# Performance work log

Measured on AMD Instinct MI355X. Metric: run time of the kernel, lower is better.

## Reference

```python
import jax, jax.numpy as jnp
import numpy as np

S = 2048      # seq_len (prefill, empty cache)
H = 32        # num query heads
HKV = 8       # num kv heads
D = 128       # head_dim
G = H // HKV  # GQA group size
SCALE = 0.08838834764831845  # 1/sqrt(D)


def setup_inputs() -> dict:
    key = jax.random.key(0)
    k1, k2, k3 = jax.random.split(key, 3)
    return {
        "query": jax.random.normal(k1, (S, H * D), dtype=jnp.float32),
        "key": jax.random.normal(k2, (S, HKV * D), dtype=jnp.float32),
        "value": jax.random.normal(k3, (S, HKV * D), dtype=jnp.float32),
    }


def reference(query, key, value):
    # [S, H, D] -> [HKV, G, S, D]; head h attends to kv head h // G,
    # equivalent to torch repeat_interleave on kv heads without materializing copies.
    q = query.reshape(S, H, D).transpose(1, 0, 2).reshape(HKV, G, S, D)
    k = key.reshape(S, HKV, D).transpose(1, 0, 2)    # [HKV, S, D]
    v = value.reshape(S, HKV, D).transpose(1, 0, 2)  # [HKV, S, D]

    scores = jnp.einsum('hgqd,htd->hgqt', q, k) * SCALE  # [HKV, G, S, S]
    causal = jnp.tril(jnp.ones((S, S), dtype=bool))      # j <= i allowed
    scores = jnp.where(causal, scores, jnp.finfo(scores.dtype).min)
    attn = jax.nn.softmax(scores, axis=-1)
    out = jnp.einsum('hgqt,htd->hgqd', attn, v)          # [HKV, G, S, D]
    out = out.reshape(H, S, D).transpose(1, 0, 2).reshape(S, H * D)
    return out
```

## Files before the change

kernel.cpp:

```cpp
#include <hip/hip_runtime.h>
#include <hip/hip_bf16.h>

#define S_LEN 2048
#define NH    32
#define NKV   8
#define HD    128
#define QBLK  128
#define KVBLK 64
#define NWAVE 8
#define KST   136
#define VST   68
#define PST   72

typedef __bf16 bf16x8   __attribute__((ext_vector_type(8)));
typedef __bf16 bf16x4_t __attribute__((ext_vector_type(4)));
typedef float  f32x4    __attribute__((ext_vector_type(4)));

__global__ __launch_bounds__(512, 4)
void sdpa_fwd(const float* __restrict__ Q, const float* __restrict__ K,
              const float* __restrict__ V, float* __restrict__ O)
{
    __shared__ __align__(16) unsigned short Klds_u[KVBLK * KST];
    __shared__ __align__(16) unsigned short Vt_u[HD * VST];
    __shared__ __align__(16) unsigned short P_u[QBLK * PST];
    __bf16* Klds = (__bf16*)Klds_u;
    __bf16* Vt   = (__bf16*)Vt_u;
    __bf16* Pl   = (__bf16*)P_u;

    const int qt   = (int)gridDim.x - 1 - (int)blockIdx.x;
    const int h    = blockIdx.y;
    const int hkv  = h >> 2;
    const int q0   = qt * QBLK;
    const int tid  = threadIdx.x;
    const int wv   = tid >> 6;
    const int lane = tid & 63;
    const int lr   = lane & 15;
    const int lg   = lane >> 4;
    const int qrow0 = q0 + wv * 16;

    const float NEG_INF = -__builtin_inff();
    const float QSCALE  = (float)(0.08838834764831845 * 1.4426950408889634);

    bf16x8 qf[4];
    {
        const float* qp = Q + (size_t)(qrow0 + lr) * (NH * HD) + h * HD + lg * 8;
        #pragma unroll
        for (int f = 0; f < 4; ++f) {
            float4 a = *(const float4*)(qp + f * 32);
            float4 b = *(const float4*)(qp + f * 32 + 4);
            bf16x8 t;
            t[0] = (__bf16)(a.x * QSCALE); t[1] = (__bf16)(a.y * QSCALE);
            t[2] = (__bf16)(a.z * QSCALE); t[3] = (__bf16)(a.w * QSCALE);
            t[4] = (__bf16)(b.x * QSCALE); t[5] = (__bf16)(b.y * QSCALE);
            t[6] = (__bf16)(b.z * QSCALE); t[7] = (__bf16)(b.w * QSCALE);
            qf[f] = t;
        }
    }

    f32x4 o[8];
    #pragma unroll
    for (int dt = 0; dt < 8; ++dt) o[dt] = (f32x4){0.f, 0.f, 0.f, 0.f};
    float m_r[4] = {NEG_INF, NEG_INF, NEG_INF, NEG_INF};
    float l_r[4] = {0.f, 0.f, 0.f, 0.f};

    const int kb_end = q0 + QBLK - KVBLK;
    for (int kb = 0; kb <= kb_end; kb += KVBLK) {
        __syncthreads();
        #pragma unroll
        for (int it = 0; it < 4; ++it) {
            int idx = (it * 512 + tid) * 4;
            int row = idx >> 7, col = idx & 127;
            float4 k4 = *(const float4*)(K + (size_t)(kb + row) * (NKV * HD) + hkv * HD + col);
            bf16x4_t kb4;
            kb4[0] = (__bf16)k4.x; kb4[1] = (__bf16)k4.y;
            kb4[2] = (__bf16)k4.z; kb4[3] = (__bf16)k4.w;
            *(bf16x4_t*)&Klds[row * KST + col] = kb4;
        }
        #pragma unroll
        for (int it = 0; it < 4; ++it) {
            int task = it * 512 + tid;
            int col = task & 127, rg = task >> 7;
            const float* vp = V + (size_t)(kb + rg * 4) * (NKV * HD) + hkv * HD + col;
            bf16x4_t vb;
            vb[0] = (__bf16)vp[0];
            vb[1] = (__bf16)vp[NKV * HD];
            vb[2] = (__bf16)vp[2 * NKV * HD];
            vb[3] = (__bf16)vp[3 * NKV * HD];
            *(bf16x4_t*)&Vt[col * VST + rg * 4] = vb;
        }
        __syncthreads();

        if (kb > qrow0 + 15) continue;

        f32x4 s[4];
        #pragma unroll
        for (int t = 0; t < 4; ++t) {
            f32x4 acc = (f32x4){0.f, 0.f, 0.f, 0.f};
            #pragma unroll
            for (int f = 0; f < 4; ++f) {
                bf16x8 kf = *(bf16x8*)&Klds[(t * 16 + lr) * KST + f * 32 + lg * 8];
                acc = __builtin_amdgcn_mfma_f32_16x16x32_bf16(qf[f], kf, acc, 0, 0, 0);
            }
            s[t] = acc;
        }

        const bool needmask = (kb + KVBLK - 1 > qrow0);
        float sv[4][4];
        float mt[4] = {NEG_INF, NEG_INF, NEG_INF, NEG_INF};
        #pragma unroll
        for (int t = 0; t < 4; ++t)
            #pragma unroll
            for (int r = 0; r < 4; ++r) {
                float val = s[t][r];
                if (needmask && (kb + t * 16 + lr) > (qrow0 + lg * 4 + r)) val = NEG_INF;
                sv[t][r] = val;
                mt[r] = fmaxf(mt[r], val);
            }
        #pragma unroll
        for (int r = 0; r < 4; ++r) {
            #pragma unroll
            for (int off = 1; off < 16; off <<= 1)
                mt[r] = fmaxf(mt[r], __shfl_xor(mt[r], off));
        }
        float alpha[4];
        #pragma unroll
        for (int r = 0; r < 4; ++r) {
            float mn  = fmaxf(m_r[r], mt[r]);
            alpha[r]  = __builtin_amdgcn_exp2f(m_r[r] - mn);
            m_r[r]    = mn;
            l_r[r]   *= alpha[r];
        }
        #pragma unroll
        for (int dt = 0; dt < 8; ++dt) {
            o[dt][0] *= alpha[0]; o[dt][1] *= alpha[1];
            o[dt][2] *= alpha[2]; o[dt][3] *= alpha[3];
        }
        #pragma unroll
        for (int t = 0; t < 4; ++t)
            #pragma unroll
            for (int r = 0; r < 4; ++r) {
                float p = __builtin_amdgcn_exp2f(sv[t][r] - m_r[r]);
                l_r[r] += p;
                Pl[(wv * 16 + lg * 4 + r) * PST + t * 16 + lr] = (__bf16)p;
            }
        #pragma unroll
        for (int ks = 0; ks < 2; ++ks) {
            bf16x8 pf = *(bf16x8*)&Pl[(wv * 16 + lr) * PST + ks * 32 + lg * 8];
            #pragma unroll
            for (int dt = 0; dt < 8; ++dt) {
                bf16x8 vf = *(bf16x8*)&Vt[(dt * 16 + lr) * VST + ks * 32 + lg * 8];
                o[dt] = __builtin_amdgcn_mfma_f32_16x16x32_bf16(pf, vf, o[dt], 0, 0, 0);
            }
        }
    }

    float inv[4];
    #pragma unroll
    for (int r = 0; r < 4; ++r) {
        float lsum = l_r[r];
        #pragma unroll
        for (int off = 1; off < 16; off <<= 1)
            lsum += __shfl_xor(lsum, off);
        inv[r] = 1.0f / lsum;
    }
    #pragma unroll
    for (int dt = 0; dt < 8; ++dt)
        #pragma unroll
        for (int r = 0; r < 4; ++r) {
            int qrow = qrow0 + lg * 4 + r;
            O[(size_t)qrow * (NH * HD) + h * HD + dt * 16 + lr] = o[dt][r] * inv[r];
        }
}

extern "C" void kernel_launch(void* const* d_in, const int* in_sizes, int n_in,
                              void* d_out, int out_size, void* d_ws, size_t ws_size,
                              hipStream_t stream)
{
    const float* Q = (const float*)d_in[0];
    const float* K = (const float*)d_in[1];
    const float* V = (const float*)d_in[2];
    float* O = (float*)d_out;
    dim3 grid(S_LEN / QBLK, NH);
    sdpa_fwd<<<grid, 512, 0, stream>>>(Q, K, V, O);
}
```

Measured before the change: 395.1 us.

## Pair causal query tiles per block and prefetch next KV tile into registers

Each block now handles two 64-row query chunks, one from the start and one from the end of the sequence, so every block has about the same causal work instead of the triangular imbalance of the old grid. It also prefetches the next K/V tile from global memory into registers while the current tile is computed, then converts and writes it to LDS after a barrier. The cost is extra registers for the prefetch buffers (16 float4-equivalents per thread), which may reduce occupancy under launch_bounds(512,4). The first-chunk waves idle through most of the loop iterations.

```diff
diff --git a/kernel.cpp b/kernel.cpp
--- a/kernel.cpp
+++ b/kernel.cpp
@@ -5,9 +5,7 @@
 #define NH    32
 #define NKV   8
 #define HD    128
-#define QBLK  128
 #define KVBLK 64
-#define NWAVE 8
 #define KST   136
 #define VST   68
 #define PST   72
@@ -22,21 +20,21 @@
 {
     __shared__ __align__(16) unsigned short Klds_u[KVBLK * KST];
     __shared__ __align__(16) unsigned short Vt_u[HD * VST];
-    __shared__ __align__(16) unsigned short P_u[QBLK * PST];
+    __shared__ __align__(16) unsigned short P_u[128 * PST];
     __bf16* Klds = (__bf16*)Klds_u;
     __bf16* Vt   = (__bf16*)Vt_u;
     __bf16* Pl   = (__bf16*)P_u;
 
-    const int qt   = (int)gridDim.x - 1 - (int)blockIdx.x;
+    const int p    = blockIdx.x;
     const int h    = blockIdx.y;
     const int hkv  = h >> 2;
-    const int q0   = qt * QBLK;
     const int tid  = threadIdx.x;
     const int wv   = tid >> 6;
     const int lane = tid & 63;
     const int lr   = lane & 15;
     const int lg   = lane >> 4;
-    const int qrow0 = q0 + wv * 16;
+    const int qrow0 = (wv < 4) ? (64 * p + 16 * wv)
+                               : (S_LEN - 64 * (p + 1) + 16 * (wv - 4));
 
     const float NEG_INF = -__builtin_inff();
     const float QSCALE  = (float)(0.08838834764831845 * 1.4426950408889634);
@@ -63,95 +61,122 @@
     float m_r[4] = {NEG_INF, NEG_INF, NEG_INF, NEG_INF};
     float l_r[4] = {0.f, 0.f, 0.f, 0.f};
 
-    const int kb_end = q0 + QBLK - KVBLK;
-    for (int kb = 0; kb <= kb_end; kb += KVBLK) {
-        __syncthreads();
+    float4 kreg[4];
+    float  vreg[16];
+
+    auto issue_loads = [&](int kb) {
         #pragma unroll
         for (int it = 0; it < 4; ++it) {
             int idx = (it * 512 + tid) * 4;
             int row = idx >> 7, col = idx & 127;
-            float4 k4 = *(const float4*)(K + (size_t)(kb + row) * (NKV * HD) + hkv * HD + col);
-            bf16x4_t kb4;
-            kb4[0] = (__bf16)k4.x; kb4[1] = (__bf16)k4.y;
-            kb4[2] = (__bf16)k4.z; kb4[3] = (__bf16)k4.w;
-            *(bf16x4_t*)&Klds[row * KST + col] = kb4;
+            kreg[it] = *(const float4*)(K + (size_t)(kb + row) * (NKV * HD) + hkv * HD + col);
         }
         #pragma unroll
         for (int it = 0; it < 4; ++it) {
             int task = it * 512 + tid;
             int col = task & 127, rg = task >> 7;
             const float* vp = V + (size_t)(kb + rg * 4) * (NKV * HD) + hkv * HD + col;
+            vreg[it * 4 + 0] = vp[0];
+            vreg[it * 4 + 1] = vp[NKV * HD];
+            vreg[it * 4 + 2] = vp[2 * NKV * HD];
+            vreg[it * 4 + 3] = vp[3 * NKV * HD];
+        }
+    };
+    auto write_lds = [&]() {
+        #pragma unroll
+        for (int it = 0; it < 4; ++it) {
+            int idx = (it * 512 + tid) * 4;
+            int row = idx >> 7, col = idx & 127;
+            bf16x4_t kb4;
+            kb4[0] = (__bf16)kreg[it].x; kb4[1] = (__bf16)kreg[it].y;
+            kb4[2] = (__bf16)kreg[it].z; kb4[3] = (__bf16)kreg[it].w;
+            *(bf16x4_t*)&Klds[row * KST + col] = kb4;
+        }
+        #pragma unroll
+        for (int it = 0; it < 4; ++it) {
+            int task = it * 512 + tid;
+            int col = task & 127, rg = task >> 7;
             bf16x4_t vb;
-            vb[0] = (__bf16)vp[0];
-            vb[1] = (__bf16)vp[NKV * HD];
-            vb[2] = (__bf16)vp[2 * NKV * HD];
-            vb[3] = (__bf16)vp[3 * NKV * HD];
+            vb[0] = (__bf16)vreg[it * 4 + 0]; vb[1] = (__bf16)vreg[it * 4 + 1];
+            vb[2] = (__bf16)vreg[it * 4 + 2]; vb[3] = (__bf16)vreg[it * 4 + 3];
             *(bf16x4_t*)&Vt[col * VST + rg * 4] = vb;
         }
+    };
+
+    const int kb_end = S_LEN - KVBLK * (p + 1);
+    issue_loads(0);
+    write_lds();
+
+    for (int kb = 0; kb <= kb_end; kb += KVBLK) {
         __syncthreads();
-
-        if (kb > qrow0 + 15) continue;
-
-        f32x4 s[4];
-        #pragma unroll
-        for (int t = 0; t < 4; ++t) {
-            f32x4 acc = (f32x4){0.f, 0.f, 0.f, 0.f};
-            #pragma unroll
-            for (int f = 0; f < 4; ++f) {
-                bf16x8 kf = *(bf16x8*)&Klds[(t * 16 + lr) * KST + f * 32 + lg * 8];
-                acc = __builtin_amdgcn_mfma_f32_16x16x32_bf16(qf[f], kf, acc, 0, 0, 0);
-            }
-            s[t] = acc;
-        }
-
-        const bool needmask = (kb + KVBLK - 1 > qrow0);
-        float sv[4][4];
-        float mt[4] = {NEG_INF, NEG_INF, NEG_INF, NEG_INF};
-        #pragma unroll
-        for (int t = 0; t < 4; ++t)
+        const bool havenext = (kb + KVBLK <= kb_end);
+        if (havenext) issue_loads(kb + KVBLK);
+
+        if (kb <= qrow0 + 15) {
+            f32x4 s[4];
+            #pragma unroll
+            for (int t = 0; t < 4; ++t) {
+                f32x4 acc = (f32x4){0.f, 0.f, 0.f, 0.f};
+                #pragma unroll
+                for (int f = 0; f < 4; ++f) {
+                    bf16x8 kf = *(bf16x8*)&Klds[(t * 16 + lr) * KST + f * 32 + lg * 8];
+                    acc = __builtin_amdgcn_mfma_f32_16x16x32_bf16(qf[f], kf, acc, 0, 0, 0);
+                }
+                s[t] = acc;
+            }
+
+            const bool needmask = (kb + KVBLK - 1 > qrow0);
+            float sv[4][4];
+            float mt[4] = {NEG_INF, NEG_INF, NEG_INF, NEG_INF};
+            #pragma unroll
+            for (int t = 0; t < 4; ++t)
+                #pragma unroll
+                for (int r = 0; r < 4; ++r) {
+                    float val = s[t][r];
+                    if (needmask && (kb + t * 16 + lr) > (qrow0 + lg * 4 + r)) val = NEG_INF;
+                    sv[t][r] = val;
+                    mt[r] = fmaxf(mt[r], val);
+                }
             #pragma unroll
             for (int r = 0; r < 4; ++r) {
-                float val = s[t][r];
-                if (needmask && (kb + t * 16 + lr) > (qrow0 + lg * 4 + r)) val = NEG_INF;
-                sv[t][r] = val;
-                mt[r] = fmaxf(mt[r], val);
-            }
-        #pragma unroll
-        for (int r = 0; r < 4; ++r) {
-            #pragma unroll
-            for (int off = 1; off < 16; off <<= 1)
-                mt[r] = fmaxf(mt[r], __shfl_xor(mt[r], off));
-        }
-        float alpha[4];
-        #pragma unroll
-        for (int r = 0; r < 4; ++r) {
-            float mn  = fmaxf(m_r[r], mt[r]);
-            alpha[r]  = __builtin_amdgcn_exp2f(m_r[r] - mn);
-            m_r[r]    = mn;
-            l_r[r]   *= alpha[r];
-        }
-        #pragma unroll
-        for (int dt = 0; dt < 8; ++dt) {
-            o[dt][0] *= alpha[0]; o[dt][1] *= alpha[1];
-            o[dt][2] *= alpha[2]; o[dt][3] *= alpha[3];
-        }
-        #pragma unroll
-        for (int t = 0; t < 4; ++t)
+                #pragma unroll
+                for (int off = 1; off < 16; off <<= 1)
+                    mt[r] = fmaxf(mt[r], __shfl_xor(mt[r], off));
+            }
+            float alpha[4];
             #pragma unroll
             for (int r = 0; r < 4; ++r) {
-                float p = __builtin_amdgcn_exp2f(sv[t][r] - m_r[r]);
-                l_r[r] += p;
-                Pl[(wv * 16 + lg * 4 + r) * PST + t * 16 + lr] = (__bf16)p;
-            }
-        #pragma unroll
-        for (int ks = 0; ks < 2; ++ks) {
-            bf16x8 pf = *(bf16x8*)&Pl[(wv * 16 + lr) * PST + ks * 32 + lg * 8];
+                float mn  = fmaxf(m_r[r], mt[r]);
+                alpha[r]  = __builtin_amdgcn_exp2f(m_r[r] - mn);
+                m_r[r]    = mn;
+                l_r[r]   *= alpha[r];
+            }
             #pragma unroll
             for (int dt = 0; dt < 8; ++dt) {
-                bf16x8 vf = *(bf16x8*)&Vt[(dt * 16 + lr) * VST + ks * 32 + lg * 8];
-                o[dt] = __builtin_amdgcn_mfma_f32_16x16x32_bf16(pf, vf, o[dt], 0, 0, 0);
-            }
-        }
+                o[dt][0] *= alpha[0]; o[dt][1] *= alpha[1];
+                o[dt][2] *= alpha[2]; o[dt][3] *= alpha[3];
+            }
+            #pragma unroll
+            for (int t = 0; t < 4; ++t)
+                #pragma unroll
+                for (int r = 0; r < 4; ++r) {
+                    float pv = __builtin_amdgcn_exp2f(sv[t][r] - m_r[r]);
+                    l_r[r] += pv;
+                    Pl[(wv * 16 + lg * 4 + r) * PST + t * 16 + lr] = (__bf16)pv;
+                }
+            #pragma unroll
+            for (int ks = 0; ks < 2; ++ks) {
+                bf16x8 pf = *(bf16x8*)&Pl[(wv * 16 + lr) * PST + ks * 32 + lg * 8];
+                #pragma unroll
+                for (int dt = 0; dt < 8; ++dt) {
+                    bf16x8 vf = *(bf16x8*)&Vt[(dt * 16 + lr) * VST + ks * 32 + lg * 8];
+                    o[dt] = __builtin_amdgcn_mfma_f32_16x16x32_bf16(pf, vf, o[dt], 0, 0, 0);
+                }
+            }
+        }
+
+        __syncthreads();
+        if (havenext) write_lds();
     }
 
     float inv[4];
@@ -180,6 +205,6 @@
     const float* K = (const float*)d_in[1];
     const float* V = (const float*)d_in[2];
     float* O = (float*)d_out;
-    dim3 grid(S_LEN / QBLK, NH);
+    dim3 grid(S_LEN / 128, NH);
     sdpa_fwd<<<grid, 512, 0, stream>>>(Q, K, V, O);
 }
```

Measured after the change: 336.3 us. 14.9% less time.
